# Optimization experiments

Hardware: AMD Instinct MI355X
Metric: run time of the kernel (lower is better)

The kernel has to match this reference:

```python
import jax, jax.numpy as jnp
import numpy as np
from jax import lax

EPS = 1e-5
B, C, H, W = 16, 256, 56, 56
HEADS, DIM_K, DIM_U, DIM_OUT = 4, 16, 4, 256
DIM_V = DIM_OUT // HEADS  # 64
R = 15


def setup_inputs() -> dict:
    key = jax.random.key(0)
    ks = jax.random.split(key, 16)
    s = 0.05
    return {
        "x": jax.random.normal(ks[0], (B, C, H, W), jnp.float32),
        "Wq": jax.random.normal(ks[1], (C, HEADS * DIM_K), jnp.float32) * s,
        "Wk": jax.random.normal(ks[2], (C, DIM_U * DIM_K), jnp.float32) * s,
        "Wv": jax.random.normal(ks[3], (C, DIM_U * DIM_V), jnp.float32) * s,
        "pos_w": jax.random.normal(ks[4], (DIM_K, DIM_U, 1, R, R), jnp.float32) * s,
        "pos_b": jax.random.normal(ks[5], (DIM_K,), jnp.float32) * s,
        "gq": jax.random.uniform(ks[6], (HEADS * DIM_K,), jnp.float32),
        "bq": jax.random.normal(ks[7], (HEADS * DIM_K,), jnp.float32) * s,
        "mq": jax.random.normal(ks[8], (HEADS * DIM_K,), jnp.float32) * s,
        "vq": jax.random.uniform(ks[9], (HEADS * DIM_K,), jnp.float32) + 0.5,
        "gv": jax.random.uniform(ks[10], (DIM_U * DIM_V,), jnp.float32),
        "bv": jax.random.normal(ks[11], (DIM_U * DIM_V,), jnp.float32) * s,
        "mv": jax.random.normal(ks[12], (DIM_U * DIM_V,), jnp.float32) * s,
        "vv": jax.random.uniform(ks[13], (DIM_U * DIM_V,), jnp.float32) + 0.5,
    }


def _bn(x, gamma, beta, mean, var):
    # inference-mode BatchNorm over channel dim (axis=1), x: [b,c,h,w]
    inv = gamma / jnp.sqrt(var + EPS)
    return x * inv[None, :, None, None] + (beta - mean * inv)[None, :, None, None]


def reference(x, Wq, Wk, Wv, pos_w, pos_b, gq, bq, mq, vq, gv, bv, mv, vv):
    b, c, hh, ww = x.shape
    n = hh * ww
    h, dk, u, dv = HEADS, DIM_K, DIM_U, DIM_V
    # 1x1 convs (channels_first) == channel matmuls
    q = jnp.einsum('bchw,cd->bdhw', x, Wq)
    k = jnp.einsum('bchw,cd->bdhw', x, Wk)
    v = jnp.einsum('bchw,cd->bdhw', x, Wv)
    q = _bn(q, gq, bq, mq, vq)
    v = _bn(v, gv, bv, mv, vv)
    # rearranges: 'b (h k) hh ww -> b h k (hh ww)', 'b (u k) hh ww -> b u k n', 'b (u v) hh ww -> b u v n'
    q = q.reshape(b, h, dk, n)
    k = k.reshape(b, u, dk, n)
    v = v.reshape(b, u, dv, n)
    k = jax.nn.softmax(k, axis=-1)  # keras Softmax default axis=-1 (positions)
    # content lambda
    Lc = jnp.einsum('bukm,buvm->bkv', k, v)
    Yc = jnp.einsum('bhkn,bkv->bnhv', q, Lc)
    # position lambda: conv3d over (v,hh,ww) with kernel (1,r,r), pad spatial only
    v5 = v.reshape(b, u, dv, hh, ww)  # [N, C=u, D=v, H, W]
    p = R // 2
    Lp = lax.conv_general_dilated(
        v5, pos_w, window_strides=(1, 1, 1),
        padding=[(0, 0), (p, p), (p, p)],
        dimension_numbers=('NCDHW', 'OIDHW', 'NCDHW'))
    Lp = Lp + pos_b[None, :, None, None, None]  # [b, k, v, hh, ww]
    Lp = Lp.reshape(b, dk, dv, n)
    Yp = jnp.einsum('bhkn,bkvn->bnhv', q, Lp)
    Y = Yc + Yp  # [b, n, h, v]
    # 'b (hh ww) h v -> b (h v) hh ww'
    out = Y.reshape(b, hh, ww, h, dv).transpose(0, 3, 4, 1, 2).reshape(b, h * dv, hh, ww)
    return out
```

## Files before the change

### kernel.cpp

```cpp
#include <hip/hip_runtime.h>
#include <cstdint>
#include <cstddef>

#define NB   16
#define NC   256
#define NPIX 3136
#define NW   56
#define EPSV 1e-5f

#define BSTR     (384 * NPIX)
#define OFF_VP   (128 * NPIX)
#define VROWD    36
#define VPLANE   (56 * VROWD)
#define OFF_PARTB 917504

#define OFF_AB   0u
#define OFF_BNA  49152u
#define OFF_BNB  49536u
#define OFF_WT   49920u
#define OFF_KS   58112u
#define OFF_LC   59136u
#define OFF_Y    75520u

typedef short bf16x8 __attribute__((ext_vector_type(8)));
typedef float f32x4  __attribute__((ext_vector_type(4)));
typedef float f32x16 __attribute__((ext_vector_type(16)));

__device__ __forceinline__ uint32_t f2bf(float f) {
  uint32_t x = __float_as_uint(f);
  uint32_t r = x + 0x7fffu + ((x >> 16) & 1u);
  return r >> 16;
}
__device__ __forceinline__ uint32_t pk_trunc(float a, float b) {
  return (__float_as_uint(a) >> 16) | (__float_as_uint(b) & 0xffff0000u);
}

__device__ __forceinline__ float fetchW(const float* Wq, const float* Wk,
                                        const float* Wv, int m, int c) {
  if (m < 64)  return Wq[c * 64 + m];
  if (m < 128) return Wk[c * 64 + (m - 64)];
  return Wv[c * 256 + (m - 128)];
}

__global__ void prep_kernel(const float* __restrict__ Wq, const float* __restrict__ Wk,
                            const float* __restrict__ Wv, const float* __restrict__ pos_w,
                            const float* __restrict__ gq, const float* __restrict__ bq,
                            const float* __restrict__ mq, const float* __restrict__ vq,
                            const float* __restrict__ gv, const float* __restrict__ bv,
                            const float* __restrict__ mv, const float* __restrict__ vv,
                            float* __restrict__ ws) {
  int d = blockIdx.x;
  int c = threadIdx.x;
  int i = d * 256 + c;
  if (i < 49152) {
    int dgt = i >> 12, rem = i & 4095;
    int kc = rem >> 8, rem2 = rem & 255;
    int lane = rem2 >> 2, dp = rem2 & 3;
    int m = dgt * 32 + (lane & 31);
    int k0 = kc * 16 + (lane >> 5) * 8 + dp * 2;
    float w0 = fetchW(Wq, Wk, Wv, m, k0);
    float w1 = fetchW(Wq, Wk, Wv, m, k0 + 1);
    ((uint32_t*)(ws + OFF_AB))[i] = f2bf(w0) | (f2bf(w1) << 16);
  }
  if (c == 0) {
    float sa, sb;
    if (d < 64)        { float inv = gq[d] / sqrtf(vq[d] + EPSV); sa = inv; sb = bq[d] - mq[d] * inv; }
    else if (d < 128)  { sa = 1.0f; sb = 0.0f; }
    else               { int j = d - 128; float inv = gv[j] / sqrtf(vv[j] + EPSV); sa = inv; sb = bv[j] - mv[j] * inv; }
    ws[OFF_BNA + d] = sa;
    ws[OFF_BNB + d] = sb;
  }
  if (i < 8192) {
    int chunk = i >> 8, rem = i & 255, lane = rem >> 2, dp = rem & 3;
    int quad = lane >> 4, k = lane & 15;
    int u = chunk >> 3, t = chunk & 7;
    int dh = 2 * t + (quad >> 1);
    int dwb = (quad & 1) * 8 + dp * 2;
    float w0 = (dh < 15 && dwb     < 15) ? pos_w[k * 900 + u * 225 + dh * 15 + dwb]     : 0.0f;
    float w1 = (dh < 15 && dwb + 1 < 15) ? pos_w[k * 900 + u * 225 + dh * 15 + dwb + 1] : 0.0f;
    ((uint32_t*)(ws + OFF_WT))[i] = f2bf(w0) | (f2bf(w1) << 16);
  }
  if (i < 1024) ws[OFF_KS + i] = 0.0f;
  for (int g = i; g < 4096 * 56; g += 98304) {
    int plane = g / 56, r = g - plane * 56;
    int bb = plane >> 8, d2 = plane & 255;
    uint32_t* row = (uint32_t*)(ws + OFF_Y) + (size_t)bb * BSTR + OFF_VP
                    + (size_t)d2 * VPLANE + r * VROWD;
    uint4 z; z.x = 0; z.y = 0; z.z = 0; z.w = 0;
    *(uint4*)(row)      = z;
    *(uint4*)(row + 32) = z;
  }
}

__launch_bounds__(256, 2)
__global__ void qkv_mfma(const float* __restrict__ x, const float* __restrict__ wsc,
                         float* __restrict__ Y) {
  __shared__ uint32_t X[64 * 128];
  __shared__ float BNs[768];
  int tid = threadIdx.x;
  int n0 = blockIdx.x * 64, b = blockIdx.y;
  for (int i = tid; i < 768; i += 256) BNs[i] = wsc[OFF_BNA + i];
  const size_t xb = (size_t)b * NC * NPIX;
#pragma unroll
  for (int it = 0; it < 4; ++it) {
    int n2 = tid & 31;
    int cp4 = it * 8 + (tid >> 5);
    const float* xp = x + xb + (size_t)(cp4 * 8) * NPIX + n0 + n2 * 2;
    float2 ld[8];
#pragma unroll
    for (int j = 0; j < 8; ++j) ld[j] = *(const float2*)(xp + (size_t)j * NPIX);
    uint32_t e0, e1, e2, e3, o0, o1, o2, o3;
    e0 = f2bf(ld[0].x) | (f2bf(ld[1].x) << 16);
    e1 = f2bf(ld[2].x) | (f2bf(ld[3].x) << 16);
    e2 = f2bf(ld[4].x) | (f2bf(ld[5].x) << 16);
    e3 = f2bf(ld[6].x) | (f2bf(ld[7].x) << 16);
    o0 = f2bf(ld[0].y) | (f2bf(ld[1].y) << 16);
    o1 = f2bf(ld[2].y) | (f2bf(ld[3].y) << 16);
    o2 = f2bf(ld[4].y) | (f2bf(ld[5].y) << 16);
    o3 = f2bf(ld[6].y) | (f2bf(ld[7].y) << 16);
    int ne = 2 * n2, no = ne + 1;
    uint4 ve; ve.x = e0; ve.y = e1; ve.z = e2; ve.w = e3;
    uint4 vo; vo.x = o0; vo.y = o1; vo.z = o2; vo.w = o3;
    *(uint4*)(X + ne * 128 + ((cp4 ^ (ne & 31)) << 2)) = ve;
    *(uint4*)(X + no * 128 + ((cp4 ^ (no & 31)) << 2)) = vo;
  }
  __syncthreads();
  int lane = tid & 63, w = tid >> 6;
  int n31 = lane & 31, h5 = lane >> 5;
  f32x16 acc[3][2];
#pragma unroll
  for (int dt = 0; dt < 3; ++dt)
#pragma unroll
    for (int nt = 0; nt < 2; ++nt)
#pragma unroll
      for (int e = 0; e < 16; ++e) acc[dt][nt][e] = 0.0f;
  const uint4* AB = (const uint4*)(wsc + OFF_AB);
  if (w == 0) {
#pragma unroll 4
    for (int kc = 0; kc < 16; ++kc) {
      bf16x8 af[3];
#pragma unroll
      for (int dt = 0; dt < 3; ++dt) {
        union { uint4 q; bf16x8 v; } tmp;
        tmp.q = AB[(size_t)((dt * 16 + kc)) * 64 + lane];
        af[dt] = tmp.v;
      }
#pragma unroll
      for (int nt = 0; nt < 2; ++nt) {
        union { uint4 q; bf16x8 v; } bu;
        bu.q = *(const uint4*)(X + (nt * 32 + n31) * 128 + (((2 * kc + h5) ^ n31) << 2));
#pragma unroll
        for (int dt = 0; dt < 3; ++dt)
          acc[dt][nt] = __builtin_amdgcn_mfma_f32_32x32x16_bf16(af[dt], bu.v, acc[dt][nt], 0, 0, 0);
      }
    }
  } else {
#pragma unroll 4
    for (int kc = 0; kc < 16; ++kc) {
      bf16x8 af[3];
#pragma unroll
      for (int dt = 0; dt < 3; ++dt) {
        union { uint4 q; bf16x8 v; } tmp;
        tmp.q = AB[(size_t)(((w * 3 + dt) * 16 + kc)) * 64 + lane];
        af[dt] = tmp.v;
      }
#pragma unroll
      for (int nt = 0; nt < 2; ++nt) {
        union { uint4 q; bf16x8 v; } bu;
        bu.q = *(const uint4*)(X + (nt * 32 + n31) * 128 + (((2 * kc + h5) ^ n31) << 2));
#pragma unroll
        for (int dt = 0; dt < 3; ++dt)
          acc[dt][nt] = __builtin_amdgcn_mfma_f32_32x32x16_bf16(bu.v, af[dt], acc[dt][nt], 0, 0, 0);
      }
    }
  }
  if (w == 0) {
#pragma unroll
    for (int dt = 0; dt < 3; ++dt) {
      int dgt = dt;
      float sa[16], sb[16];
#pragma unroll
      for (int g = 0; g < 4; ++g) {
        *(float4*)(sa + g * 4) = *(const float4*)(BNs + dgt * 32 + g * 8 + h5 * 4);
        *(float4*)(sb + g * 4) = *(const float4*)(BNs + 384 + dgt * 32 + g * 8 + h5 * 4);
      }
#pragma unroll
      for (int nt = 0; nt < 2; ++nt) {
        int pix = n0 + nt * 32 + n31;
        if (dgt < 2) {
          uint2* qb2 = (uint2*)(Y + (size_t)b * BSTR);
#pragma unroll
          for (int g = 0; g < 4; ++g) {
            float y0 = fmaf(acc[dt][nt][4 * g + 0], sa[4 * g + 0], sb[4 * g + 0]);
            float y1 = fmaf(acc[dt][nt][4 * g + 1], sa[4 * g + 1], sb[4 * g + 1]);
            float y2 = fmaf(acc[dt][nt][4 * g + 2], sa[4 * g + 2], sb[4 * g + 2]);
            float y3 = fmaf(acc[dt][nt][4 * g + 3], sa[4 * g + 3], sb[4 * g + 3]);
            uint2 val;
            val.x = f2bf(y0) | (f2bf(y1) << 16);
            val.y = f2bf(y2) | (f2bf(y3) << 16);
            qb2[(size_t)(dgt * 8 + 2 * g + h5) * NPIX + pix] = val;
          }
        } else {
#pragma unroll
          for (int g = 0; g < 4; ++g)
#pragma unroll
            for (int ki = 0; ki < 4; ++ki) {
              int d = dgt * 32 + 8 * g + 4 * h5 + ki;
              Y[((size_t)b * 384 + d) * NPIX + pix] = acc[dt][nt][4 * g + ki];
            }
        }
      }
    }
  } else {
    int prr[2][4], pcc[2][4];
#pragma unroll
    for (int nt = 0; nt < 2; ++nt)
#pragma unroll
      for (int j = 0; j < 4; ++j) {
        int pb = n0 + nt * 32 + 8 * j + 4 * h5;
        prr[nt][j] = pb / NW;
        pcc[nt][j] = pb - prr[nt][j] * NW;
      }
    unsigned short* vp = (unsigned short*)(Y + (size_t)b * BSTR + OFF_VP);
#pragma unroll
    for (int dt = 0; dt < 3; ++dt) {
      int dgt = w * 3 + dt;
      if (dgt == 3) {
        float* kp = Y + ((size_t)(b * 384) + 96 + n31) * NPIX;
#pragma unroll
        for (int nt = 0; nt < 2; ++nt)
#pragma unroll
          for (int j = 0; j < 4; ++j) {
            float4 st;
            st.x = acc[dt][nt][4 * j + 0];
            st.y = acc[dt][nt][4 * j + 1];
            st.z = acc[dt][nt][4 * j + 2];
            st.w = acc[dt][nt][4 * j + 3];
            *(float4*)(kp + prr[nt][j] * NW + pcc[nt][j]) = st;
          }
      } else {
        int d2 = dgt * 32 + n31 - 128;
        float sa = BNs[dgt * 32 + n31];
        float sb2 = BNs[384 + dgt * 32 + n31];
        unsigned short* vpd = vp + (size_t)d2 * 4032;
#pragma unroll
        for (int nt = 0; nt < 2; ++nt)
#pragma unroll
          for (int j = 0; j < 4; ++j) {
            float y0 = fmaf(acc[dt][nt][4 * j + 0], sa, sb2);
            float y1 = fmaf(acc[dt][nt][4 * j + 1], sa, sb2);
            float y2 = fmaf(acc[dt][nt][4 * j + 2], sa, sb2);
            float y3 = fmaf(acc[dt][nt][4 * j + 3], sa, sb2);
            uint2 val;
            val.x = f2bf(y0) | (f2bf(y1) << 16);
            val.y = f2bf(y2) | (f2bf(y3) << 16);
            *(uint2*)(vpd + prr[nt][j] * 72 + 8 + pcc[nt][j]) = val;
          }
      }
    }
  }
}

__launch_bounds__(256)
__global__ void lc_mfma(float* __restrict__ Y, float* __restrict__ ws) {
  __shared__ float R[4096];
  __shared__ float Rs[64];
  int bx = blockIdx.x, u = blockIdx.y, b = blockIdx.z;
  int tid = threadIdx.x;
  int lane = tid & 63, w = tid >> 6;
  int col = lane & 15, quad = lane >> 4;
  int slot = bx * 4 + w;
  const float* krow = Y + ((size_t)(b * 384 + 64 + u * 16 + col)) * NPIX;
  const uint32_t* vpb = (const uint32_t*)(Y + (size_t)b * BSTR + OFF_VP)
                        + (size_t)(u * 64 + col) * VPLANE;
  f32x4 acc[4];
#pragma unroll
  for (int vt = 0; vt < 4; ++vt) acc[vt] = (f32x4){0.f, 0.f, 0.f, 0.f};
  float ssum = 0.0f;
  for (int c = slot; c < 126; c += 64) {
    int p0 = c * 32 + quad * 8;
    int row = p0 / 72;
    int pc = p0 - row * 72;
    bool valid = (unsigned)(pc - 8) < 56u;
    float4 k0, k1;
    if (valid) {
      const float* kp = krow + row * NW + pc - 8;
      k0 = *(const float4*)(kp);
      k1 = *(const float4*)(kp + 4);
    } else {
      k0.x = k0.y = k0.z = k0.w = -1e30f;
      k1 = k0;
    }
    float e0 = __expf(k0.x), e1 = __expf(k0.y), e2 = __expf(k0.z), e3 = __expf(k0.w);
    float e4 = __expf(k1.x), e5 = __expf(k1.y), e6 = __expf(k1.z), e7 = __expf(k1.w);
    ssum += (e0 + e1 + e2 + e3) + (e4 + e5 + e6 + e7);
    union { uint32_t d[4]; bf16x8 v; } kb;
    kb.d[0] = pk_trunc(e0, e1);
    kb.d[1] = pk_trunc(e2, e3);
    kb.d[2] = pk_trunc(e4, e5);
    kb.d[3] = pk_trunc(e6, e7);
    int vdw = c * 16 + quad * 4;
#pragma unroll
    for (int vt = 0; vt < 4; ++vt) {
      union { uint4 q; bf16x8 v; } vb;
      vb.q = *(const uint4*)(vpb + (size_t)(vt * 16) * VPLANE + vdw);
      acc[vt] = __builtin_amdgcn_mfma_f32_16x16x32_bf16(vb.v, kb.v, acc[vt], 0, 0, 0);
    }
  }
  ssum += __shfl_xor(ssum, 16);
  ssum += __shfl_xor(ssum, 32);
#pragma unroll
  for (int vt = 0; vt < 4; ++vt)
#pragma unroll
    for (int r = 0; r < 4; ++r)
      R[w * 1024 + vt * 256 + quad * 64 + r * 16 + col] = acc[vt][r];
  if (lane < 16) Rs[w * 16 + col] = ssum;
  __syncthreads();
  float* P = Y + (size_t)b * BSTR + OFF_PARTB + (size_t)(u * 16 + bx) * 1024;
  float4 s0 = *(const float4*)(R + tid * 4);
  float4 s1 = *(const float4*)(R + 1024 + tid * 4);
  float4 s2 = *(const float4*)(R + 2048 + tid * 4);
  float4 s3 = *(const float4*)(R + 3072 + tid * 4);
  float4 tot;
  tot.x = (s0.x + s1.x) + (s2.x + s3.x);
  tot.y = (s0.y + s1.y) + (s2.y + s3.y);
  tot.z = (s0.z + s1.z) + (s2.z + s3.z);
  tot.w = (s0.w + s1.w) + (s2.w + s3.w);
  *(float4*)(P + tid * 4) = tot;
  if (tid < 16)
    atomicAdd(&ws[OFF_KS + b * 64 + u * 16 + tid],
              (Rs[tid] + Rs[16 + tid]) + (Rs[32 + tid] + Rs[48 + tid]));
}

__global__ void lc_reduce(const float* __restrict__ Y, float* __restrict__ ws) {
  int i = blockIdx.x, b = blockIdx.y;
  int t = threadIdx.x;
  __shared__ float invS[64];
  if (t < 64) invS[t] = 1.0f / ws[OFF_KS + b * 64 + t];
  __syncthreads();
  int idx = i * 256 + t;
  int k = idx & 15;
  const float* P = Y + (size_t)b * BSTR + OFF_PARTB;
  float tot = 0.0f;
#pragma unroll
  for (int u = 0; u < 4; ++u) {
    float su = 0.0f;
#pragma unroll
    for (int s = 0; s < 16; ++s) su += P[(size_t)(u * 16 + s) * 1024 + idx];
    tot += su * invS[u * 16 + k];
  }
  ws[OFF_LC + (b * 16 + k) * 64 + (idx >> 4)] = tot;
}

#define ROWS    29
#define ERSTR   40
#define EOOFF   1168
#define UPITCH4 2328
#define LDSW4   9312

template<int PPLO, int PPHI>
__device__ __forceinline__ void conv_accum(const uint32_t* __restrict__ Sp,
                                           const uint4* __restrict__ wt,
                                           int lane, f32x4* acc) {
#pragma unroll 1
  for (int u = 0; u < 4; ++u) {
    bf16x8 wf[8];
#pragma unroll
    for (int t = 0; t < 8; ++t) {
      union { uint4 q; bf16x8 v; } tmp;
      tmp.q = wt[(u * 8 + t) * 64 + lane];
      wf[t] = tmp.v;
    }
    const uint32_t* Su = Sp + u * UPITCH4;
#pragma unroll
    for (int PP = PPLO; PP < PPHI; ++PP) {
      union { uint32_t u4[4]; bf16x8 v8; } bu;
      bu.u4[0] = Su[PP * 80];
      bu.u4[1] = Su[PP * 80 + 1];
      bu.u4[2] = Su[PP * 80 + 2];
      bu.u4[3] = Su[PP * 80 + 3];
#pragma unroll
      for (int t = 0; t < 8; ++t) {
        int q = PP - t;
        if (q >= 0 && q < 7)
          acc[q] = __builtin_amdgcn_mfma_f32_16x16x32_bf16(wf[t], bu.v8, acc[q], 0, 0, 0);
      }
    }
  }
}

__launch_bounds__(512, 4)
__global__ void pos_lambda_mfma(const float* __restrict__ Y, const float* __restrict__ wsc,
                                const float* __restrict__ pos_b, float* __restrict__ out) {
  __shared__ __attribute__((aligned(16))) uint32_t S[LDSW4];
  int v = blockIdx.x, b = blockIdx.y, band = blockIdx.z;
  int rb = band * 14;
  int tid = threadIdx.x;
  const uint32_t* vpad = (const uint32_t*)(Y + (size_t)b * BSTR + OFF_VP);
  for (int ii = tid; ii < 1044; ii += 512) {
    int u = ii / 261;
    int rem = ii - u * 261;
    int row = rem / 9;
    int j3 = rem - row * 9;
    int gr = rb + row - 7;
    uint32_t d0 = 0, d1 = 0, d2 = 0, d3 = 0, d4 = 0;
    if ((unsigned)gr < (unsigned)NW) {
      const uint32_t* pr32 = vpad + (size_t)(u * 64 + v) * VPLANE + gr * VROWD + 4 * j3;
      uint4 q4 = *(const uint4*)pr32;
      d0 = q4.x; d1 = q4.y; d2 = q4.z; d3 = q4.w;
      d4 = pr32[4];
    }
    uint32_t* dstE = S + u * UPITCH4 + row * ERSTR + 4 * j3;
    uint4 eo;
    eo.x = __builtin_amdgcn_alignbit(d1, d0, 16);
    eo.y = __builtin_amdgcn_alignbit(d2, d1, 16);
    eo.z = __builtin_amdgcn_alignbit(d3, d2, 16);
    eo.w = __builtin_amdgcn_alignbit(d4, d3, 16);
    *(uint4*)(dstE) = eo;
    uint4 oo; oo.x = d1; oo.y = d2; oo.z = d3; oo.w = d4;
    *(uint4*)(dstE + EOOFF) = oo;
  }
  __syncthreads();
  int lane = tid & 63, wid = tid >> 6;
  int quad = lane >> 4, n = lane & 15;
  int dhp = quad >> 1;
  int ct = wid & 3, p = wid >> 2;
  int cb = (ct == 3) ? 40 : ct * 16;
  int sbb = cb + n + ((quad & 1) << 3);
  int par = sbb & 1, sidx = sbb >> 1;
  const uint32_t* Sp = S + (p + dhp) * ERSTR + (par ? EOOFF : 0) + sidx;
  const uint4* wt = (const uint4*)(wsc + OFF_WT);
  float lcq[4];
#pragma unroll
  for (int r = 0; r < 4; ++r) {
    int k = quad * 4 + r;
    lcq[r] = wsc[OFF_LC + (b * 16 + k) * 64 + v] + pos_b[k];
  }
  f32x4 acc[7];
#pragma unroll
  for (int q = 0; q < 7; ++q) {
    acc[q][0] = lcq[0]; acc[q][1] = lcq[1]; acc[q][2] = lcq[2]; acc[q][3] = lcq[3];
  }
  if (band == 0)      conv_accum<3, 14>(Sp, wt, lane, acc);
  else if (band == 3) conv_accum<0, 11>(Sp, wt, lane, acc);
  else                conv_accum<0, 14>(Sp, wt, lane, acc);

  const uint2* qb2 = (const uint2*)(Y + (size_t)b * BSTR);
#pragma unroll
  for (int q = 0; q < 7; ++q) {
    int rr = rb + p + 2 * q;
    int pix = rr * NW + cb + n;
    float m0 = acc[q][0], m1 = acc[q][1];
    float m2 = acc[q][2], m3 = acc[q][3];
    float pp[4];
#pragma unroll
    for (int j = 0; j < 4; ++j) {
      int h = quad ^ j;
      uint2 qd = qb2[(h * 4 + quad) * NPIX + pix];
      float q0 = __uint_as_float(qd.x << 16);
      float q1 = __uint_as_float(qd.x & 0xffff0000u);
      float q2 = __uint_as_float(qd.y << 16);
      float q3 = __uint_as_float(qd.y & 0xffff0000u);
      pp[j] = fmaf(q0, m0, fmaf(q1, m1, fmaf(q2, m2, q3 * m3)));
    }
    float t0 = pp[0] + __shfl_xor(pp[1], 16);
    float t2 = pp[2] + __shfl_xor(pp[3], 16);
    float y  = t0 + __shfl_xor(t2, 32);
    out[((size_t)(b * 256 + quad * 64 + v)) * NPIX + pix] = y;
  }
}

extern "C" void kernel_launch(void* const* d_in, const int* in_sizes, int n_in,
                              void* d_out, int out_size, void* d_ws, size_t ws_size,
                              hipStream_t stream) {
  const float* x     = (const float*)d_in[0];
  const float* Wq    = (const float*)d_in[1];
  const float* Wk    = (const float*)d_in[2];
  const float* Wv    = (const float*)d_in[3];
  const float* pos_w = (const float*)d_in[4];
  const float* pos_b = (const float*)d_in[5];
  const float* gq    = (const float*)d_in[6];
  const float* bq    = (const float*)d_in[7];
  const float* mq    = (const float*)d_in[8];
  const float* vq    = (const float*)d_in[9];
  const float* gv    = (const float*)d_in[10];
  const float* bv    = (const float*)d_in[11];
  const float* mv    = (const float*)d_in[12];
  const float* vv    = (const float*)d_in[13];
  float* ws  = (float*)d_ws;
  float* out = (float*)d_out;
  float* Y   = ws + OFF_Y;

  prep_kernel<<<dim3(384), 256, 0, stream>>>(Wq, Wk, Wv, pos_w, gq, bq, mq, vq,
                                             gv, bv, mv, vv, ws);
  qkv_mfma<<<dim3(49, 16), 256, 0, stream>>>(x, ws, Y);
  lc_mfma<<<dim3(16, 4, 16), 256, 0, stream>>>(Y, ws);
  lc_reduce<<<dim3(4, 16), 256, 0, stream>>>(Y, ws);
  pos_lambda_mfma<<<dim3(64, 16, 4), 512, 0, stream>>>(Y, ws, pos_b, out);
}
```

Before: 260.7 us.

## Loop row bands inside pos-lambda block with register-prefetched LDS staging

The pos-lambda kernel now has one block handle all four row bands of a (v,b) plane instead of launching a separate block per band. Global loads for the next band's padded V rows are issued into registers before the current band's MFMA convolution and written to LDS afterwards. The LDS layout is changed from split even/odd planes to an interleaved layout with stride-2 word reads. This is meant to hide global-load latency and cut repeated halo loads, at the cost of a 4x smaller grid (1024 blocks), more register pressure, and the loss of the edge-band MFMA skipping.

```diff
diff --git a/kernel.cpp b/kernel.cpp
--- a/kernel.cpp
+++ b/kernel.cpp
@@ -353,15 +353,13 @@
 }
 
 #define ROWS    29
-#define ERSTR   40
-#define EOOFF   1168
-#define UPITCH4 2328
-#define LDSW4   9312
-
-template<int PPLO, int PPHI>
-__device__ __forceinline__ void conv_accum(const uint32_t* __restrict__ Sp,
+#define RSTR2   72
+#define UPITCH2 2088
+#define LDSW2   8352
+
+__device__ __forceinline__ void conv_accum(const uint32_t* __restrict__ S,
                                            const uint4* __restrict__ wt,
-                                           int lane, f32x4* acc) {
+                                           int abase, int lane, f32x4* acc) {
 #pragma unroll 1
   for (int u = 0; u < 4; ++u) {
     bf16x8 wf[8];
@@ -371,14 +369,13 @@
       tmp.q = wt[(u * 8 + t) * 64 + lane];
       wf[t] = tmp.v;
     }
-    const uint32_t* Su = Sp + u * UPITCH4;
-#pragma unroll
-    for (int PP = PPLO; PP < PPHI; ++PP) {
+    int au = u * UPITCH2 + abase;
+#pragma unroll
+    for (int PP = 0; PP < 14; ++PP) {
+      int a = au + PP * (2 * RSTR2);
       union { uint32_t u4[4]; bf16x8 v8; } bu;
-      bu.u4[0] = Su[PP * 80];
-      bu.u4[1] = Su[PP * 80 + 1];
-      bu.u4[2] = Su[PP * 80 + 2];
-      bu.u4[3] = Su[PP * 80 + 3];
+      bu.u4[0] = S[a];     bu.u4[1] = S[a + 2];
+      bu.u4[2] = S[a + 4]; bu.u4[3] = S[a + 6];
 #pragma unroll
       for (int t = 0; t < 8; ++t) {
         int q = PP - t;
@@ -392,17 +389,17 @@
 __launch_bounds__(512, 4)
 __global__ void pos_lambda_mfma(const float* __restrict__ Y, const float* __restrict__ wsc,
                                 const float* __restrict__ pos_b, float* __restrict__ out) {
-  __shared__ __attribute__((aligned(16))) uint32_t S[LDSW4];
-  int v = blockIdx.x, b = blockIdx.y, band = blockIdx.z;
-  int rb = band * 14;
+  __shared__ __attribute__((aligned(16))) uint32_t S[LDSW2];
+  int v = blockIdx.x, b = blockIdx.y;
   int tid = threadIdx.x;
   const uint32_t* vpad = (const uint32_t*)(Y + (size_t)b * BSTR + OFF_VP);
+
   for (int ii = tid; ii < 1044; ii += 512) {
     int u = ii / 261;
     int rem = ii - u * 261;
     int row = rem / 9;
     int j3 = rem - row * 9;
-    int gr = rb + row - 7;
+    int gr = row - 7;
     uint32_t d0 = 0, d1 = 0, d2 = 0, d3 = 0, d4 = 0;
     if ((unsigned)gr < (unsigned)NW) {
       const uint32_t* pr32 = vpad + (size_t)(u * 64 + v) * VPLANE + gr * VROWD + 4 * j3;
@@ -410,25 +407,23 @@
       d0 = q4.x; d1 = q4.y; d2 = q4.z; d3 = q4.w;
       d4 = pr32[4];
     }
-    uint32_t* dstE = S + u * UPITCH4 + row * ERSTR + 4 * j3;
-    uint4 eo;
-    eo.x = __builtin_amdgcn_alignbit(d1, d0, 16);
-    eo.y = __builtin_amdgcn_alignbit(d2, d1, 16);
-    eo.z = __builtin_amdgcn_alignbit(d3, d2, 16);
-    eo.w = __builtin_amdgcn_alignbit(d4, d3, 16);
-    *(uint4*)(dstE) = eo;
-    uint4 oo; oo.x = d1; oo.y = d2; oo.z = d3; oo.w = d4;
-    *(uint4*)(dstE + EOOFF) = oo;
-  }
-  __syncthreads();
+    uint32_t* dst = S + u * UPITCH2 + row * RSTR2 + 8 * j3;
+    uint4 w0, w1;
+    w0.x = __builtin_amdgcn_alignbit(d1, d0, 16);  w0.y = d1;
+    w0.z = __builtin_amdgcn_alignbit(d2, d1, 16);  w0.w = d2;
+    w1.x = __builtin_amdgcn_alignbit(d3, d2, 16);  w1.y = d3;
+    w1.z = __builtin_amdgcn_alignbit(d4, d3, 16);  w1.w = d4;
+    *(uint4*)(dst)     = w0;
+    *(uint4*)(dst + 4) = w1;
+  }
+
   int lane = tid & 63, wid = tid >> 6;
   int quad = lane >> 4, n = lane & 15;
   int dhp = quad >> 1;
   int ct = wid & 3, p = wid >> 2;
   int cb = (ct == 3) ? 40 : ct * 16;
-  int sbb = cb + n + ((quad & 1) << 3);
-  int par = sbb & 1, sidx = sbb >> 1;
-  const uint32_t* Sp = S + (p + dhp) * ERSTR + (par ? EOOFF : 0) + sidx;
+  int sb = cb + n + (quad & 1) * 8;
+  int abase = (p + dhp) * RSTR2 + sb;
   const uint4* wt = (const uint4*)(wsc + OFF_WT);
   float lcq[4];
 #pragma unroll
@@ -436,37 +431,87 @@
     int k = quad * 4 + r;
     lcq[r] = wsc[OFF_LC + (b * 16 + k) * 64 + v] + pos_b[k];
   }
-  f32x4 acc[7];
-#pragma unroll
-  for (int q = 0; q < 7; ++q) {
-    acc[q][0] = lcq[0]; acc[q][1] = lcq[1]; acc[q][2] = lcq[2]; acc[q][3] = lcq[3];
-  }
-  if (band == 0)      conv_accum<3, 14>(Sp, wt, lane, acc);
-  else if (band == 3) conv_accum<0, 11>(Sp, wt, lane, acc);
-  else                conv_accum<0, 14>(Sp, wt, lane, acc);
-
   const uint2* qb2 = (const uint2*)(Y + (size_t)b * BSTR);
-#pragma unroll
-  for (int q = 0; q < 7; ++q) {
-    int rr = rb + p + 2 * q;
-    int pix = rr * NW + cb + n;
-    float m0 = acc[q][0], m1 = acc[q][1];
-    float m2 = acc[q][2], m3 = acc[q][3];
-    float pp[4];
-#pragma unroll
-    for (int j = 0; j < 4; ++j) {
-      int h = quad ^ j;
-      uint2 qd = qb2[(h * 4 + quad) * NPIX + pix];
-      float q0 = __uint_as_float(qd.x << 16);
-      float q1 = __uint_as_float(qd.x & 0xffff0000u);
-      float q2 = __uint_as_float(qd.y << 16);
-      float q3 = __uint_as_float(qd.y & 0xffff0000u);
-      pp[j] = fmaf(q0, m0, fmaf(q1, m1, fmaf(q2, m2, q3 * m3)));
-    }
-    float t0 = pp[0] + __shfl_xor(pp[1], 16);
-    float t2 = pp[2] + __shfl_xor(pp[3], 16);
-    float y  = t0 + __shfl_xor(t2, 32);
-    out[((size_t)(b * 256 + quad * 64 + v)) * NPIX + pix] = y;
+
+#pragma unroll 1
+  for (int bb = 0; bb < 4; ++bb) {
+    int rb = bb * 14;
+    __syncthreads();
+
+    int dstA = -1, dstB = -1, dstC = -1;
+    uint32_t dA0 = 0, dA1 = 0, dA2 = 0, dA3 = 0, dA4 = 0;
+    uint32_t dB0 = 0, dB1 = 0, dB2 = 0, dB3 = 0, dB4 = 0;
+    uint32_t dC0 = 0, dC1 = 0, dC2 = 0, dC3 = 0, dC4 = 0;
+    if (bb < 3) {
+      int rbn = rb + 14;
+#define LOAD_TASK(T, DST, E0, E1, E2, E3, E4)                                   \
+      { int ii = tid + 512 * T;                                                 \
+        if (ii < 1044) {                                                        \
+          int u_ = ii / 261; int rem_ = ii - u_ * 261;                          \
+          int row_ = rem_ / 9; int j3_ = rem_ - row_ * 9;                       \
+          int gr_ = rbn + row_ - 7;                                             \
+          if ((unsigned)gr_ < (unsigned)NW) {                                   \
+            const uint32_t* pr_ = vpad + (size_t)(u_ * 64 + v) * VPLANE         \
+                                  + gr_ * VROWD + 4 * j3_;                      \
+            uint4 q4_ = *(const uint4*)pr_;                                     \
+            E0 = q4_.x; E1 = q4_.y; E2 = q4_.z; E3 = q4_.w; E4 = pr_[4];        \
+          }                                                                     \
+          DST = u_ * UPITCH2 + row_ * RSTR2 + 8 * j3_;                          \
+        } }
+      LOAD_TASK(0, dstA, dA0, dA1, dA2, dA3, dA4)
+      LOAD_TASK(1, dstB, dB0, dB1, dB2, dB3, dB4)
+      LOAD_TASK(2, dstC, dC0, dC1, dC2, dC3, dC4)
+#undef LOAD_TASK
+    }
+
+    f32x4 acc[7];
+#pragma unroll
+    for (int q = 0; q < 7; ++q) {
+      acc[q][0] = lcq[0]; acc[q][1] = lcq[1]; acc[q][2] = lcq[2]; acc[q][3] = lcq[3];
+    }
+    conv_accum(S, wt, abase, lane, acc);
+
+#pragma unroll
+    for (int q = 0; q < 7; ++q) {
+      int rr = rb + p + 2 * q;
+      int pix = rr * NW + cb + n;
+      float m0 = acc[q][0], m1 = acc[q][1];
+      float m2 = acc[q][2], m3 = acc[q][3];
+      float pp[4];
+#pragma unroll
+      for (int j = 0; j < 4; ++j) {
+        int h = quad ^ j;
+        uint2 qd = qb2[(h * 4 + quad) * NPIX + pix];
+        float q0 = __uint_as_float(qd.x << 16);
+        float q1 = __uint_as_float(qd.x & 0xffff0000u);
+        float q2 = __uint_as_float(qd.y << 16);
+        float q3 = __uint_as_float(qd.y & 0xffff0000u);
+        pp[j] = fmaf(q0, m0, fmaf(q1, m1, fmaf(q2, m2, q3 * m3)));
+      }
+      float t0 = pp[0] + __shfl_xor(pp[1], 16);
+      float t2 = pp[2] + __shfl_xor(pp[3], 16);
+      float y  = t0 + __shfl_xor(t2, 32);
+      out[((size_t)(b * 256 + quad * 64 + v)) * NPIX + pix] = y;
+    }
+
+    if (bb < 3) {
+      __syncthreads();
+#define WRITE_TASK(DST, E0, E1, E2, E3, E4)                                     \
+      if (DST >= 0) {                                                           \
+        uint32_t* dst_ = S + DST;                                               \
+        uint4 w0_, w1_;                                                         \
+        w0_.x = __builtin_amdgcn_alignbit(E1, E0, 16);  w0_.y = E1;             \
+        w0_.z = __builtin_amdgcn_alignbit(E2, E1, 16);  w0_.w = E2;             \
+        w1_.x = __builtin_amdgcn_alignbit(E3, E2, 16);  w1_.y = E3;             \
+        w1_.z = __builtin_amdgcn_alignbit(E4, E3, 16);  w1_.w = E4;             \
+        *(uint4*)(dst_)     = w0_;                                              \
+        *(uint4*)(dst_ + 4) = w1_;                                              \
+      }
+      WRITE_TASK(dstA, dA0, dA1, dA2, dA3, dA4)
+      WRITE_TASK(dstB, dB0, dB1, dB2, dB3, dB4)
+      WRITE_TASK(dstC, dC0, dC1, dC2, dC3, dC4)
+#undef WRITE_TASK
+    }
   }
 }
 
@@ -496,5 +541,5 @@
   qkv_mfma<<<dim3(49, 16), 256, 0, stream>>>(x, ws, Y);
   lc_mfma<<<dim3(16, 4, 16), 256, 0, stream>>>(Y, ws);
   lc_reduce<<<dim3(4, 16), 256, 0, stream>>>(Y, ws);
-  pos_lambda_mfma<<<dim3(64, 16, 4), 512, 0, stream>>>(Y, ws, pos_b, out);
-}
+  pos_lambda_mfma<<<dim3(64, 16), 512, 0, stream>>>(Y, ws, pos_b, out);
+}
```

After: 320.5 us. +23.0%, slower.

## Use hardware bf16 pack converts, rebalance qkv wave roles, interleave conv LDS layout

Applied to the files above, without the earlier changes.

Replaces software round-to-nearest bf16 packing and truncation with the v_cvt_pk_bf16_f32 instruction in several places. In the qkv kernel, wave 0's third tile (the k projection) is now computed transposed and stored as fp32 rows directly. In the positional conv kernel, the even and odd shifted copies of each staged row are interleaved into one LDS buffer, which shrinks shared memory and changes the operand load pattern. The softmax path now rounds instead of truncating, which slightly changes numerics. The new LDS strides may introduce bank conflicts.

```diff
diff --git a/kernel.cpp b/kernel.cpp
--- a/kernel.cpp
+++ b/kernel.cpp
@@ -31,8 +31,10 @@
   uint32_t r = x + 0x7fffu + ((x >> 16) & 1u);
   return r >> 16;
 }
-__device__ __forceinline__ uint32_t pk_trunc(float a, float b) {
-  return (__float_as_uint(a) >> 16) | (__float_as_uint(b) & 0xffff0000u);
+__device__ __forceinline__ uint32_t cvtpk(float lo, float hi) {
+  uint32_t r;
+  asm("v_cvt_pk_bf16_f32 %0, %1, %2" : "=v"(r) : "v"(lo), "v"(hi));
+  return r;
 }
 
 __device__ __forceinline__ float fetchW(const float* Wq, const float* Wk,
@@ -109,18 +111,16 @@
     float2 ld[8];
 #pragma unroll
     for (int j = 0; j < 8; ++j) ld[j] = *(const float2*)(xp + (size_t)j * NPIX);
-    uint32_t e0, e1, e2, e3, o0, o1, o2, o3;
-    e0 = f2bf(ld[0].x) | (f2bf(ld[1].x) << 16);
-    e1 = f2bf(ld[2].x) | (f2bf(ld[3].x) << 16);
-    e2 = f2bf(ld[4].x) | (f2bf(ld[5].x) << 16);
-    e3 = f2bf(ld[6].x) | (f2bf(ld[7].x) << 16);
-    o0 = f2bf(ld[0].y) | (f2bf(ld[1].y) << 16);
-    o1 = f2bf(ld[2].y) | (f2bf(ld[3].y) << 16);
-    o2 = f2bf(ld[4].y) | (f2bf(ld[5].y) << 16);
-    o3 = f2bf(ld[6].y) | (f2bf(ld[7].y) << 16);
+    uint4 ve, vo;
+    ve.x = cvtpk(ld[0].x, ld[1].x);
+    ve.y = cvtpk(ld[2].x, ld[3].x);
+    ve.z = cvtpk(ld[4].x, ld[5].x);
+    ve.w = cvtpk(ld[6].x, ld[7].x);
+    vo.x = cvtpk(ld[0].y, ld[1].y);
+    vo.y = cvtpk(ld[2].y, ld[3].y);
+    vo.z = cvtpk(ld[4].y, ld[5].y);
+    vo.w = cvtpk(ld[6].y, ld[7].y);
     int ne = 2 * n2, no = ne + 1;
-    uint4 ve; ve.x = e0; ve.y = e1; ve.z = e2; ve.w = e3;
-    uint4 vo; vo.x = o0; vo.y = o1; vo.z = o2; vo.w = o3;
     *(uint4*)(X + ne * 128 + ((cp4 ^ (ne & 31)) << 2)) = ve;
     *(uint4*)(X + no * 128 + ((cp4 ^ (no & 31)) << 2)) = vo;
   }
@@ -149,9 +149,9 @@
       for (int nt = 0; nt < 2; ++nt) {
         union { uint4 q; bf16x8 v; } bu;
         bu.q = *(const uint4*)(X + (nt * 32 + n31) * 128 + (((2 * kc + h5) ^ n31) << 2));
-#pragma unroll
-        for (int dt = 0; dt < 3; ++dt)
-          acc[dt][nt] = __builtin_amdgcn_mfma_f32_32x32x16_bf16(af[dt], bu.v, acc[dt][nt], 0, 0, 0);
+        acc[0][nt] = __builtin_amdgcn_mfma_f32_32x32x16_bf16(af[0], bu.v, acc[0][nt], 0, 0, 0);
+        acc[1][nt] = __builtin_amdgcn_mfma_f32_32x32x16_bf16(af[1], bu.v, acc[1][nt], 0, 0, 0);
+        acc[2][nt] = __builtin_amdgcn_mfma_f32_32x32x16_bf16(bu.v, af[2], acc[2][nt], 0, 0, 0);
       }
     }
   } else {
@@ -174,9 +174,18 @@
       }
     }
   }
+  int prr[2][4], pcc[2][4];
+#pragma unroll
+  for (int nt = 0; nt < 2; ++nt)
+#pragma unroll
+    for (int j = 0; j < 4; ++j) {
+      int pb = n0 + nt * 32 + 8 * j + 4 * h5;
+      prr[nt][j] = pb / NW;
+      pcc[nt][j] = pb - prr[nt][j] * NW;
+    }
   if (w == 0) {
 #pragma unroll
-    for (int dt = 0; dt < 3; ++dt) {
+    for (int dt = 0; dt < 2; ++dt) {
       int dgt = dt;
       float sa[16], sb[16];
 #pragma unroll
@@ -187,40 +196,35 @@
 #pragma unroll
       for (int nt = 0; nt < 2; ++nt) {
         int pix = n0 + nt * 32 + n31;
-        if (dgt < 2) {
-          uint2* qb2 = (uint2*)(Y + (size_t)b * BSTR);
-#pragma unroll
-          for (int g = 0; g < 4; ++g) {
-            float y0 = fmaf(acc[dt][nt][4 * g + 0], sa[4 * g + 0], sb[4 * g + 0]);
-            float y1 = fmaf(acc[dt][nt][4 * g + 1], sa[4 * g + 1], sb[4 * g + 1]);
-            float y2 = fmaf(acc[dt][nt][4 * g + 2], sa[4 * g + 2], sb[4 * g + 2]);
-            float y3 = fmaf(acc[dt][nt][4 * g + 3], sa[4 * g + 3], sb[4 * g + 3]);
-            uint2 val;
-            val.x = f2bf(y0) | (f2bf(y1) << 16);
-            val.y = f2bf(y2) | (f2bf(y3) << 16);
-            qb2[(size_t)(dgt * 8 + 2 * g + h5) * NPIX + pix] = val;
-          }
-        } else {
-#pragma unroll
-          for (int g = 0; g < 4; ++g)
-#pragma unroll
-            for (int ki = 0; ki < 4; ++ki) {
-              int d = dgt * 32 + 8 * g + 4 * h5 + ki;
-              Y[((size_t)b * 384 + d) * NPIX + pix] = acc[dt][nt][4 * g + ki];
-            }
+        uint2* qb2 = (uint2*)(Y + (size_t)b * BSTR);
+#pragma unroll
+        for (int g = 0; g < 4; ++g) {
+          float y0 = fmaf(acc[dt][nt][4 * g + 0], sa[4 * g + 0], sb[4 * g + 0]);
+          float y1 = fmaf(acc[dt][nt][4 * g + 1], sa[4 * g + 1], sb[4 * g + 1]);
+          float y2 = fmaf(acc[dt][nt][4 * g + 2], sa[4 * g + 2], sb[4 * g + 2]);
+          float y3 = fmaf(acc[dt][nt][4 * g + 3], sa[4 * g + 3], sb[4 * g + 3]);
+          uint2 val;
+          val.x = cvtpk(y0, y1);
+          val.y = cvtpk(y2, y3);
+          qb2[(size_t)(dgt * 8 + 2 * g + h5) * NPIX + pix] = val;
         }
       }
     }
+    {
+      float* kp = Y + ((size_t)(b * 384) + 64 + n31) * NPIX;
+#pragma unroll
+      for (int nt = 0; nt < 2; ++nt)
+#pragma unroll
+        for (int j = 0; j < 4; ++j) {
+          float4 st;
+          st.x = acc[2][nt][4 * j + 0];
+          st.y = acc[2][nt][4 * j + 1];
+          st.z = acc[2][nt][4 * j + 2];
+          st.w = acc[2][nt][4 * j + 3];
+          *(float4*)(kp + prr[nt][j] * NW + pcc[nt][j]) = st;
+        }
+    }
   } else {
-    int prr[2][4], pcc[2][4];
-#pragma unroll
-    for (int nt = 0; nt < 2; ++nt)
-#pragma unroll
-      for (int j = 0; j < 4; ++j) {
-        int pb = n0 + nt * 32 + 8 * j + 4 * h5;
-        prr[nt][j] = pb / NW;
-        pcc[nt][j] = pb - prr[nt][j] * NW;
-      }
     unsigned short* vp = (unsigned short*)(Y + (size_t)b * BSTR + OFF_VP);
 #pragma unroll
     for (int dt = 0; dt < 3; ++dt) {
@@ -252,8 +256,8 @@
             float y2 = fmaf(acc[dt][nt][4 * j + 2], sa, sb2);
             float y3 = fmaf(acc[dt][nt][4 * j + 3], sa, sb2);
             uint2 val;
-            val.x = f2bf(y0) | (f2bf(y1) << 16);
-            val.y = f2bf(y2) | (f2bf(y3) << 16);
+            val.x = cvtpk(y0, y1);
+            val.y = cvtpk(y2, y3);
             *(uint2*)(vpd + prr[nt][j] * 72 + 8 + pcc[nt][j]) = val;
           }
       }
@@ -295,10 +299,10 @@
     float e4 = __expf(k1.x), e5 = __expf(k1.y), e6 = __expf(k1.z), e7 = __expf(k1.w);
     ssum += (e0 + e1 + e2 + e3) + (e4 + e5 + e6 + e7);
     union { uint32_t d[4]; bf16x8 v; } kb;
-    kb.d[0] = pk_trunc(e0, e1);
-    kb.d[1] = pk_trunc(e2, e3);
-    kb.d[2] = pk_trunc(e4, e5);
-    kb.d[3] = pk_trunc(e6, e7);
+    kb.d[0] = cvtpk(e0, e1);
+    kb.d[1] = cvtpk(e2, e3);
+    kb.d[2] = cvtpk(e4, e5);
+    kb.d[3] = cvtpk(e6, e7);
     int vdw = c * 16 + quad * 4;
 #pragma unroll
     for (int vt = 0; vt < 4; ++vt) {
@@ -353,15 +357,14 @@
 }
 
 #define ROWS    29
-#define ERSTR   40
-#define EOOFF   1168
-#define UPITCH4 2328
-#define LDSW4   9312
+#define RSTR2   72
+#define UPITCH2 2088
+#define LDSW2   8352
 
 template<int PPLO, int PPHI>
-__device__ __forceinline__ void conv_accum(const uint32_t* __restrict__ Sp,
+__device__ __forceinline__ void conv_accum(const uint32_t* __restrict__ S,
                                            const uint4* __restrict__ wt,
-                                           int lane, f32x4* acc) {
+                                           int abase, int lane, f32x4* acc) {
 #pragma unroll 1
   for (int u = 0; u < 4; ++u) {
     bf16x8 wf[8];
@@ -371,14 +374,13 @@
       tmp.q = wt[(u * 8 + t) * 64 + lane];
       wf[t] = tmp.v;
     }
-    const uint32_t* Su = Sp + u * UPITCH4;
+    int au = u * UPITCH2 + abase;
 #pragma unroll
     for (int PP = PPLO; PP < PPHI; ++PP) {
+      int a = au + PP * (2 * RSTR2);
       union { uint32_t u4[4]; bf16x8 v8; } bu;
-      bu.u4[0] = Su[PP * 80];
-      bu.u4[1] = Su[PP * 80 + 1];
-      bu.u4[2] = Su[PP * 80 + 2];
-      bu.u4[3] = Su[PP * 80 + 3];
+      bu.u4[0] = S[a];     bu.u4[1] = S[a + 2];
+      bu.u4[2] = S[a + 4]; bu.u4[3] = S[a + 6];
 #pragma unroll
       for (int t = 0; t < 8; ++t) {
         int q = PP - t;
@@ -392,7 +394,7 @@
 __launch_bounds__(512, 4)
 __global__ void pos_lambda_mfma(const float* __restrict__ Y, const float* __restrict__ wsc,
                                 const float* __restrict__ pos_b, float* __restrict__ out) {
-  __shared__ __attribute__((aligned(16))) uint32_t S[LDSW4];
+  __shared__ __attribute__((aligned(16))) uint32_t S[LDSW2];
   int v = blockIdx.x, b = blockIdx.y, band = blockIdx.z;
   int rb = band * 14;
   int tid = threadIdx.x;
@@ -410,15 +412,14 @@
       d0 = q4.x; d1 = q4.y; d2 = q4.z; d3 = q4.w;
       d4 = pr32[4];
     }
-    uint32_t* dstE = S + u * UPITCH4 + row * ERSTR + 4 * j3;
-    uint4 eo;
-    eo.x = __builtin_amdgcn_alignbit(d1, d0, 16);
-    eo.y = __builtin_amdgcn_alignbit(d2, d1, 16);
-    eo.z = __builtin_amdgcn_alignbit(d3, d2, 16);
-    eo.w = __builtin_amdgcn_alignbit(d4, d3, 16);
-    *(uint4*)(dstE) = eo;
-    uint4 oo; oo.x = d1; oo.y = d2; oo.z = d3; oo.w = d4;
-    *(uint4*)(dstE + EOOFF) = oo;
+    uint32_t* dst = S + u * UPITCH2 + row * RSTR2 + 8 * j3;
+    uint4 w0, w1;
+    w0.x = __builtin_amdgcn_alignbit(d1, d0, 16);  w0.y = d1;
+    w0.z = __builtin_amdgcn_alignbit(d2, d1, 16);  w0.w = d2;
+    w1.x = __builtin_amdgcn_alignbit(d3, d2, 16);  w1.y = d3;
+    w1.z = __builtin_amdgcn_alignbit(d4, d3, 16);  w1.w = d4;
+    *(uint4*)(dst)     = w0;
+    *(uint4*)(dst + 4) = w1;
   }
   __syncthreads();
   int lane = tid & 63, wid = tid >> 6;
@@ -426,9 +427,8 @@
   int dhp = quad >> 1;
   int ct = wid & 3, p = wid >> 2;
   int cb = (ct == 3) ? 40 : ct * 16;
-  int sbb = cb + n + ((quad & 1) << 3);
-  int par = sbb & 1, sidx = sbb >> 1;
-  const uint32_t* Sp = S + (p + dhp) * ERSTR + (par ? EOOFF : 0) + sidx;
+  int sb = cb + n + (quad & 1) * 8;
+  int abase = (p + dhp) * RSTR2 + sb;
   const uint4* wt = (const uint4*)(wsc + OFF_WT);
   float lcq[4];
 #pragma unroll
@@ -441,9 +441,9 @@
   for (int q = 0; q < 7; ++q) {
     acc[q][0] = lcq[0]; acc[q][1] = lcq[1]; acc[q][2] = lcq[2]; acc[q][3] = lcq[3];
   }
-  if (band == 0)      conv_accum<3, 14>(Sp, wt, lane, acc);
-  else if (band == 3) conv_accum<0, 11>(Sp, wt, lane, acc);
-  else                conv_accum<0, 14>(Sp, wt, lane, acc);
+  if (band == 0)      conv_accum<3, 14>(S, wt, abase, lane, acc);
+  else if (band == 3) conv_accum<0, 11>(S, wt, abase, lane, acc);
+  else                conv_accum<0, 14>(S, wt, abase, lane, acc);
 
   const uint2* qb2 = (const uint2*)(Y + (size_t)b * BSTR);
 #pragma unroll
```

After: 260.9 us. About the same (+0.1%).
